# Optimization experiments

Hardware: AMD Instinct MI355X
Metric: run time of the kernel (lower is better)

The kernel has to match this reference:

```python
import jax, jax.numpy as jnp
import numpy as np

N = 100000      # nodes
E = 3200000     # edges
F_IN = 9        # atom features
H = 128         # hidden_dim
L = 4           # num_layers
G = 512         # graphs in batch
BN_EPS = 1e-5


def setup_inputs() -> dict:
    key = jax.random.key(0)
    ks = jax.random.split(key, 24)
    s = 0.05
    inp = {}
    inp["x"] = jax.random.normal(ks[0], (N, F_IN), jnp.float32)
    inp["edge_index"] = jax.random.randint(ks[1], (2, E), 0, N, dtype=jnp.int64)
    inp["batch"] = jnp.sort(jax.random.randint(ks[2], (N,), 0, G, dtype=jnp.int64))
    # atom embedding
    inp["Wemb"] = jax.random.normal(ks[3], (F_IN, H), jnp.float32) * s
    inp["bemb"] = jnp.zeros((H,), jnp.float32)
    # per-layer GINConv params (stacked over L layers)
    inp["eps"] = jnp.zeros((L,), jnp.float32)  # train_eps=True, init 0
    inp["W1"] = jax.random.normal(ks[4], (L, H, 2 * H), jnp.float32) * s
    inp["b1"] = jnp.zeros((L, 2 * H), jnp.float32)
    inp["g1"] = jax.random.uniform(ks[5], (L, 2 * H), jnp.float32, 0.9, 1.1)
    inp["be1"] = jax.random.normal(ks[6], (L, 2 * H), jnp.float32) * s
    inp["m1"] = jax.random.normal(ks[7], (L, 2 * H), jnp.float32) * s
    inp["v1"] = jax.random.uniform(ks[8], (L, 2 * H), jnp.float32, 0.5, 1.5)
    inp["W2"] = jax.random.normal(ks[9], (L, 2 * H, H), jnp.float32) * s
    inp["b2"] = jnp.zeros((L, H), jnp.float32)
    # outer BatchNorm per layer
    inp["g2"] = jax.random.uniform(ks[10], (L, H), jnp.float32, 0.9, 1.1)
    inp["be2"] = jax.random.normal(ks[11], (L, H), jnp.float32) * s
    inp["m2"] = jax.random.normal(ks[12], (L, H), jnp.float32) * s
    inp["v2"] = jax.random.uniform(ks[13], (L, H), jnp.float32, 0.5, 1.5)
    return inp


def _bn(x, g, b, m, v):
    # eval-mode BatchNorm1d with running stats
    return g * (x - m) * jax.lax.rsqrt(v + BN_EPS) + b


def reference(x, edge_index, batch, Wemb, bemb, eps, W1, b1, g1, be1, m1, v1,
              W2, b2, g2, be2, m2, v2):
    h = x @ Wemb + bemb                                   # [N, H]
    src, dst = edge_index[0], edge_index[1]
    for i in range(L):
        # GIN aggregation: sum of neighbor (source) features into target
        agg = jax.ops.segment_sum(h[src], dst, num_segments=N)   # [N, H]
        z = (1.0 + eps[i]) * h + agg
        # MLP: Linear -> BN -> ReLU -> Linear
        z = jax.nn.relu(_bn(z @ W1[i] + b1[i], g1[i], be1[i], m1[i], v1[i]))
        h = z @ W2[i] + b2[i]
        # outer BN + ReLU (dropout skipped: eval mode)
        h = jax.nn.relu(_bn(h, g2[i], be2[i], m2[i], v2[i]))
    # global_mean_pool
    sums = jax.ops.segment_sum(h, batch, num_segments=G)          # [G, H]
    counts = jax.ops.segment_sum(jnp.ones((N, 1), h.dtype), batch,
                                 num_segments=G)                  # [G, 1]
    return sums / jnp.maximum(counts, 1.0)
```

## Files before the change

### kernel.cpp

```cpp
#include <hip/hip_runtime.h>
#include <stdint.h>

#define H 128
#define H2 256
#define NLAYERS 4
#define BN_EPS 1e-5f

#define BSHIFT 10
#define NPB 1024
#define NBC 98
#define PART_BATCH 2048
#define EPT 8

typedef __attribute__((ext_vector_type(4))) float f32x4;
typedef __attribute__((ext_vector_type(8))) short bhalf8;

__device__ __forceinline__ float bf2f(unsigned short u) {
    union { unsigned int i; float f; } v;
    v.i = ((unsigned int)u) << 16;
    return v.f;
}
__device__ __forceinline__ unsigned short f2bf(float f) {
    union { float f; unsigned int i; } v;
    v.f = f;
    unsigned int b = v.i + 0x7FFFu + ((v.i >> 16) & 1u);
    return (unsigned short)(b >> 16);
}

__global__ __launch_bounds__(256) void embed_kernel(
    const float* __restrict__ x, const float* __restrict__ Wemb,
    const float* __restrict__ bemb, unsigned short* __restrict__ h, int N) {
    int n = blockIdx.x * 2 + (threadIdx.x >> 7);
    int f = threadIdx.x & 127;
    if (n >= N) return;
    const float* xr = x + (size_t)n * 9;
    float acc = bemb[f];
#pragma unroll
    for (int k = 0; k < 9; k++) acc += xr[k] * Wemb[k * H + f];
    h[(size_t)n * H + f] = f2bf(acc);
}

__global__ void prep_params(
    const float* __restrict__ b1, const float* __restrict__ g1, const float* __restrict__ be1,
    const float* __restrict__ m1, const float* __restrict__ v1,
    const float* __restrict__ b2, const float* __restrict__ g2, const float* __restrict__ be2,
    const float* __restrict__ m2, const float* __restrict__ v2,
    float* __restrict__ sc1, float* __restrict__ sh1,
    float* __restrict__ sc2, float* __restrict__ sh2) {
    int t = threadIdx.x;
    if (t < NLAYERS * H2) {
        float s = g1[t] * rsqrtf(v1[t] + BN_EPS);
        sc1[t] = s;
        sh1[t] = (b1[t] - m1[t]) * s + be1[t];
    }
    if (t < NLAYERS * H) {
        float s = g2[t] * rsqrtf(v2[t] + BN_EPS);
        sc2[t] = s;
        sh2[t] = (b2[t] - m2[t]) * s + be2[t];
    }
}

__global__ __launch_bounds__(256) void prep_weights(
    const float* __restrict__ W1, const float* __restrict__ W2,
    unsigned short* __restrict__ W1F, unsigned short* __restrict__ W2F) {
    int idx = blockIdx.x * 256 + threadIdx.x;
    if (idx >= NLAYERS * H * H2) return;
    {
        int e = idx & 7;
        int lane = (idx >> 3) & 63;
        int ks = (idx >> 9) & 3;
        int c16 = (idx >> 11) & 15;
        int l = idx >> 15;
        int c = c16 * 16 + (lane & 15);
        int k = ks * 32 + (lane >> 4) * 8 + e;
        W1F[idx] = f2bf(W1[((size_t)l * H + k) * H2 + c]);
    }
    {
        int e = idx & 7;
        int lane = (idx >> 3) & 63;
        int ks = (idx >> 9) & 7;
        int c16 = (idx >> 12) & 7;
        int l = idx >> 15;
        int c = c16 * 16 + (lane & 15);
        int k = ks * 32 + (lane >> 4) * 8 + e;
        W2F[idx] = f2bf(W2[((size_t)l * H2 + k) * H + c]);
    }
}

__global__ __launch_bounds__(256) void hist_coarse(const int* __restrict__ ei,
                                                   unsigned* __restrict__ bc_cnt,
                                                   int E, int nbc) {
    __shared__ unsigned lh[NBC];
    for (int i = threadIdx.x; i < nbc; i += 256) lh[i] = 0;
    __syncthreads();
    for (int e = blockIdx.x * 256 + threadIdx.x; e < E; e += gridDim.x * 256)
        atomicAdd(&lh[(unsigned)ei[E + e] >> BSHIFT], 1u);
    __syncthreads();
    for (int i = threadIdx.x; i < nbc; i += 256)
        if (lh[i]) atomicAdd(&bc_cnt[i], lh[i]);
}

__global__ __launch_bounds__(128) void scan_coarse(const unsigned* __restrict__ bc_cnt,
                                                   unsigned* __restrict__ bc_base,
                                                   unsigned* __restrict__ bc_cursor,
                                                   int nbc, int E) {
    __shared__ unsigned sd[128];
    int t = threadIdx.x;
    unsigned v = (t < nbc) ? bc_cnt[t] : 0u;
    sd[t] = v;
    __syncthreads();
    for (int off = 1; off < 128; off <<= 1) {
        unsigned xv = (t >= off) ? sd[t - off] : 0u;
        __syncthreads();
        sd[t] += xv;
        __syncthreads();
    }
    unsigned excl = sd[t] - v;
    if (t < nbc) {
        bc_base[t] = excl;
        bc_cursor[t] = excl;
    }
    if (t == 0) bc_base[nbc] = (unsigned)E;
}

__global__ __launch_bounds__(256) void partition_kernel(const int* __restrict__ ei,
                                                        unsigned* __restrict__ bc_cursor,
                                                        uint2* __restrict__ part,
                                                        int E, int nbc) {
    __shared__ unsigned lh[NBC];
    __shared__ unsigned lb[NBC];
    for (int i = threadIdx.x; i < nbc; i += 256) lh[i] = 0;
    __syncthreads();
    int base = blockIdx.x * PART_BATCH;
    int s[EPT], d[EPT];
    unsigned rank[EPT];
    int bk[EPT];
#pragma unroll
    for (int k = 0; k < EPT; k++) {
        int e = base + k * 256 + threadIdx.x;
        if (e < E) {
            s[k] = ei[e];
            d[k] = ei[E + e];
            bk[k] = (unsigned)d[k] >> BSHIFT;
            rank[k] = atomicAdd(&lh[bk[k]], 1u);
        } else bk[k] = -1;
    }
    __syncthreads();
    for (int i = threadIdx.x; i < nbc; i += 256)
        lb[i] = lh[i] ? atomicAdd(&bc_cursor[i], lh[i]) : 0u;
    __syncthreads();
#pragma unroll
    for (int k = 0; k < EPT; k++) {
        if (bk[k] >= 0) {
            unsigned p = lb[bk[k]] + rank[k];
            part[p] = make_uint2((unsigned)s[k], (unsigned)d[k]);
        }
    }
}

__global__ __launch_bounds__(1024) void bucket_degrees(const uint2* __restrict__ part,
                                                       const unsigned* __restrict__ bc_base,
                                                       unsigned* __restrict__ gdeg, int N) {
    __shared__ unsigned deg[NPB];
    int b = blockIdx.x;
    deg[threadIdx.x] = 0;
    __syncthreads();
    unsigned r0 = bc_base[b], r1 = bc_base[b + 1];
    for (unsigned i = r0 + threadIdx.x; i < r1; i += 1024)
        atomicAdd(&deg[part[i].y & (NPB - 1)], 1u);
    __syncthreads();
    int node = (b << BSHIFT) + threadIdx.x;
    if (node < N) gdeg[node] = deg[threadIdx.x];
}

__global__ __launch_bounds__(256) void scanA_kernel(const unsigned* __restrict__ deg,
                                                    unsigned* __restrict__ rowptr,
                                                    unsigned* __restrict__ bsum, int N) {
    __shared__ unsigned sd[256];
    int tid = threadIdx.x;
    int base = blockIdx.x * 1024 + tid * 4;
    unsigned v[4];
    unsigned s = 0;
#pragma unroll
    for (int j = 0; j < 4; j++) {
        v[j] = (base + j < N) ? deg[base + j] : 0u;
        s += v[j];
    }
    sd[tid] = s;
    __syncthreads();
    for (int off = 1; off < 256; off <<= 1) {
        unsigned xv = (tid >= off) ? sd[tid - off] : 0u;
        __syncthreads();
        sd[tid] += xv;
        __syncthreads();
    }
    unsigned excl = sd[tid] - s;
#pragma unroll
    for (int j = 0; j < 4; j++) {
        if (base + j < N) rowptr[base + j] = excl;
        excl += v[j];
    }
    if (tid == 255) bsum[blockIdx.x] = sd[255];
}

__global__ __launch_bounds__(1024) void scanB_kernel(unsigned* __restrict__ bsum, int nb) {
    __shared__ unsigned sd[1024];
    int t = threadIdx.x;
    unsigned s = (t < nb) ? bsum[t] : 0u;
    sd[t] = s;
    __syncthreads();
    for (int off = 1; off < 1024; off <<= 1) {
        unsigned xv = (t >= off) ? sd[t - off] : 0u;
        __syncthreads();
        sd[t] += xv;
        __syncthreads();
    }
    if (t < nb) bsum[t] = sd[t] - s;
}

__global__ __launch_bounds__(256) void scanC_kernel(unsigned* __restrict__ rowptr,
                                                    const unsigned* __restrict__ bsum,
                                                    int N, int E) {
    int base = blockIdx.x * 1024 + threadIdx.x * 4;
    unsigned off = bsum[blockIdx.x];
#pragma unroll
    for (int j = 0; j < 4; j++) {
        int i = base + j;
        if (i < N) rowptr[i] += off;
    }
    if (blockIdx.x == 0 && threadIdx.x == 0) rowptr[N] = (unsigned)E;
}

__global__ __launch_bounds__(1024) void bucket_fill(const uint2* __restrict__ part,
                                                    const unsigned* __restrict__ bc_base,
                                                    const unsigned* __restrict__ rowptr,
                                                    unsigned* __restrict__ col, int N) {
    __shared__ unsigned cur[NPB];
    int b = blockIdx.x;
    int node = (b << BSHIFT) + threadIdx.x;
    cur[threadIdx.x] = (node < N) ? rowptr[node] : 0u;
    __syncthreads();
    unsigned r0 = bc_base[b], r1 = bc_base[b + 1];
    for (unsigned i = r0 + threadIdx.x; i < r1; i += 1024) {
        uint2 e = part[i];
        unsigned p = atomicAdd(&cur[e.y & (NPB - 1)], 1u);
        col[p] = e.x;
    }
}

__global__ __launch_bounds__(256) void agg_kernel(
    const unsigned short* __restrict__ h, const unsigned* __restrict__ rowptr,
    const unsigned* __restrict__ col, const float* __restrict__ eps, int layer,
    unsigned short* __restrict__ z, int N) {
    int n = blockIdx.x * 4 + (threadIdx.x >> 6);
    if (n >= N) return;
    int lane = threadIdx.x & 63;
    int chunk = lane & 15;
    int sub = lane >> 4;
    unsigned r0 = rowptr[n], r1 = rowptr[n + 1];
    float a0[8], a1[8], a2[8], a3[8];
#pragma unroll
    for (int k = 0; k < 8; k++) { a0[k] = 0.f; a1[k] = 0.f; a2[k] = 0.f; a3[k] = 0.f; }
    unsigned j = r0 + sub;
    for (; j + 12 < r1; j += 16) {
        unsigned c0 = col[j], c1 = col[j + 4], c2 = col[j + 8], c3 = col[j + 12];
        bhalf8 v0 = *(const bhalf8*)&h[(size_t)c0 * H + chunk * 8];
        bhalf8 v1 = *(const bhalf8*)&h[(size_t)c1 * H + chunk * 8];
        bhalf8 v2 = *(const bhalf8*)&h[(size_t)c2 * H + chunk * 8];
        bhalf8 v3 = *(const bhalf8*)&h[(size_t)c3 * H + chunk * 8];
#pragma unroll
        for (int k = 0; k < 8; k++) {
            a0[k] += bf2f((unsigned short)v0[k]);
            a1[k] += bf2f((unsigned short)v1[k]);
            a2[k] += bf2f((unsigned short)v2[k]);
            a3[k] += bf2f((unsigned short)v3[k]);
        }
    }
    for (; j < r1; j += 4) {
        unsigned c0 = col[j];
        bhalf8 v0 = *(const bhalf8*)&h[(size_t)c0 * H + chunk * 8];
#pragma unroll
        for (int k = 0; k < 8; k++) a0[k] += bf2f((unsigned short)v0[k]);
    }
#pragma unroll
    for (int k = 0; k < 8; k++) {
        a0[k] += a1[k] + (a2[k] + a3[k]);
        a0[k] += __shfl_xor(a0[k], 16, 64);
        a0[k] += __shfl_xor(a0[k], 32, 64);
    }
    if (sub == 0) {
        float e = 1.0f + eps[layer];
        bhalf8 hv = *(const bhalf8*)&h[(size_t)n * H + chunk * 8];
        bhalf8 o;
#pragma unroll
        for (int k = 0; k < 8; k++)
            o[k] = (short)f2bf(e * bf2f((unsigned short)hv[k]) + a0[k]);
        *(bhalf8*)&z[(size_t)n * H + chunk * 8] = o;
    }
}

#define LDP 264
__global__ __launch_bounds__(256) void mlp_fused_kernel(
    const unsigned short* __restrict__ z, const unsigned short* __restrict__ W1F,
    const unsigned short* __restrict__ W2F,
    const float* __restrict__ sc1, const float* __restrict__ sh1,
    const float* __restrict__ sc2, const float* __restrict__ sh2,
    unsigned short* __restrict__ h, int N) {
    __shared__ unsigned short tl[64 * LDP];
    int wave = threadIdx.x >> 6, lane = threadIdx.x & 63;
    int rtile = blockIdx.x * 64;
    int rlane = lane & 15;
    int kq = lane >> 4;
    int kg = kq * 8;
    int arow[4];
#pragma unroll
    for (int rb = 0; rb < 4; rb++) {
        int r = rtile + rb * 16 + rlane;
        arow[rb] = r < N ? r : N - 1;
    }
    f32x4 zero = {0.f, 0.f, 0.f, 0.f};
    {
        f32x4 acc[4][4];
#pragma unroll
        for (int rb = 0; rb < 4; rb++)
#pragma unroll
            for (int cb = 0; cb < 4; cb++) acc[rb][cb] = zero;
#pragma unroll
        for (int ks = 0; ks < 4; ks++) {
            bhalf8 a[4], b[4];
#pragma unroll
            for (int rb = 0; rb < 4; rb++)
                a[rb] = *(const bhalf8*)&z[(size_t)arow[rb] * H + ks * 32 + kg];
#pragma unroll
            for (int cb = 0; cb < 4; cb++)
                b[cb] = *(const bhalf8*)&W1F[((size_t)((wave * 4 + cb) * 4 + ks) * 64 + lane) * 8];
#pragma unroll
            for (int rb = 0; rb < 4; rb++)
#pragma unroll
                for (int cb = 0; cb < 4; cb++)
                    acc[rb][cb] = __builtin_amdgcn_mfma_f32_16x16x32_bf16(a[rb], b[cb], acc[rb][cb], 0, 0, 0);
        }
#pragma unroll
        for (int cb = 0; cb < 4; cb++) {
            int colc = wave * 64 + cb * 16 + rlane;
            float sc = sc1[colc], sh = sh1[colc];
#pragma unroll
            for (int rb = 0; rb < 4; rb++) {
#pragma unroll
                for (int j = 0; j < 4; j++) {
                    int rl = rb * 16 + kq * 4 + j;
                    float vv = acc[rb][cb][j] * sc + sh;
                    vv = vv > 0.f ? vv : 0.f;
                    tl[rl * LDP + colc] = f2bf(vv);
                }
            }
        }
    }
    __syncthreads();
    {
        f32x4 acc[4][2];
#pragma unroll
        for (int rb = 0; rb < 4; rb++)
#pragma unroll
            for (int cb = 0; cb < 2; cb++) acc[rb][cb] = zero;
#pragma unroll
        for (int ks = 0; ks < 8; ks++) {
            bhalf8 a[4], b[2];
#pragma unroll
            for (int rb = 0; rb < 4; rb++)
                a[rb] = *(const bhalf8*)&tl[(rb * 16 + rlane) * LDP + ks * 32 + kg];
#pragma unroll
            for (int cb = 0; cb < 2; cb++)
                b[cb] = *(const bhalf8*)&W2F[((size_t)((wave * 2 + cb) * 8 + ks) * 64 + lane) * 8];
#pragma unroll
            for (int rb = 0; rb < 4; rb++)
#pragma unroll
                for (int cb = 0; cb < 2; cb++)
                    acc[rb][cb] = __builtin_amdgcn_mfma_f32_16x16x32_bf16(a[rb], b[cb], acc[rb][cb], 0, 0, 0);
        }
        int rr = rtile + kq * 4;
#pragma unroll
        for (int cb = 0; cb < 2; cb++) {
            int colc = wave * 32 + cb * 16 + rlane;
            float sc = sc2[colc], sh = sh2[colc];
#pragma unroll
            for (int rb = 0; rb < 4; rb++) {
#pragma unroll
                for (int j = 0; j < 4; j++) {
                    int row = rr + rb * 16 + j;
                    if (row < N) {
                        float vv = acc[rb][cb][j] * sc + sh;
                        vv = vv > 0.f ? vv : 0.f;
                        h[(size_t)row * H + colc] = f2bf(vv);
                    }
                }
            }
        }
    }
}

__global__ __launch_bounds__(128) void pool_kernel(
    const unsigned short* __restrict__ h, const int* __restrict__ batch,
    float* __restrict__ out, int N, int G) {
    __shared__ int se[2];
    int g = blockIdx.x;
    if (threadIdx.x == 0) {
        int lo = 0, hi = N;
        while (lo < hi) {
            int mid = (lo + hi) >> 1;
            if (batch[mid] < g) lo = mid + 1; else hi = mid;
        }
        se[0] = lo;
        hi = N;
        while (lo < hi) {
            int mid = (lo + hi) >> 1;
            if (batch[mid] < g + 1) lo = mid + 1; else hi = mid;
        }
        se[1] = lo;
    }
    __syncthreads();
    int s = se[0], e = se[1];
    int f = threadIdx.x;
    float acc = 0.f;
    for (int r = s; r < e; ++r) acc += bf2f(h[(size_t)r * H + f]);
    int cnt = e - s;
    out[(size_t)g * H + f] = cnt > 0 ? acc / (float)cnt : 0.f;
}

extern "C" void kernel_launch(void* const* d_in, const int* in_sizes, int n_in,
                              void* d_out, int out_size, void* d_ws, size_t ws_size,
                              hipStream_t stream) {
    const float* x     = (const float*)d_in[0];
    const int*   ei    = (const int*)d_in[1];
    const int*   batch = (const int*)d_in[2];
    const float* Wemb  = (const float*)d_in[3];
    const float* bemb  = (const float*)d_in[4];
    const float* eps   = (const float*)d_in[5];
    const float* W1    = (const float*)d_in[6];
    const float* b1    = (const float*)d_in[7];
    const float* g1    = (const float*)d_in[8];
    const float* be1   = (const float*)d_in[9];
    const float* m1    = (const float*)d_in[10];
    const float* v1    = (const float*)d_in[11];
    const float* W2    = (const float*)d_in[12];
    const float* b2    = (const float*)d_in[13];
    const float* g2    = (const float*)d_in[14];
    const float* be2   = (const float*)d_in[15];
    const float* m2    = (const float*)d_in[16];
    const float* v2    = (const float*)d_in[17];

    int N = in_sizes[0] / 9;
    int E = in_sizes[1] / 2;
    int G = out_size / H;
    int nbc = (N + NPB - 1) >> BSHIFT;

    char* p = (char*)d_ws;
    auto alloc = [&](size_t bytes) -> char* {
        char* r = p;
        p += (bytes + 255) & ~(size_t)255;
        return r;
    };
    unsigned short* h   = (unsigned short*)alloc((size_t)N * H * 2);
    unsigned short* z   = (unsigned short*)alloc((size_t)N * H * 2);
    uint2*          part = (uint2*)alloc((size_t)E * 8);
    unsigned*       rowptr = (unsigned*)alloc((size_t)(N + 1) * 4);
    unsigned*       gdeg   = (unsigned*)alloc((size_t)N * 4);
    unsigned*       bsum   = (unsigned*)alloc(1024 * 4);
    unsigned*       col    = (unsigned*)alloc((size_t)E * 4);
    unsigned short* W1F = (unsigned short*)alloc((size_t)NLAYERS * H * H2 * 2);
    unsigned short* W2F = (unsigned short*)alloc((size_t)NLAYERS * H * H2 * 2);
    float* sc1 = (float*)alloc(NLAYERS * H2 * 4);
    float* sh1 = (float*)alloc(NLAYERS * H2 * 4);
    float* sc2 = (float*)alloc(NLAYERS * H * 4);
    float* sh2 = (float*)alloc(NLAYERS * H * 4);
    unsigned* bc_cnt    = (unsigned*)alloc((NBC + 2) * 4);
    unsigned* bc_base   = (unsigned*)alloc((NBC + 2) * 4);
    unsigned* bc_cursor = (unsigned*)alloc((NBC + 2) * 4);

    hipMemsetAsync(bc_cnt, 0, (NBC + 2) * 4, stream);
    prep_params<<<1, 1024, 0, stream>>>(b1, g1, be1, m1, v1, b2, g2, be2, m2, v2,
                                        sc1, sh1, sc2, sh2);
    prep_weights<<<(NLAYERS * H * H2 + 255) / 256, 256, 0, stream>>>(W1, W2, W1F, W2F);
    embed_kernel<<<(N + 1) / 2, 256, 0, stream>>>(x, Wemb, bemb, h, N);

    hist_coarse<<<512, 256, 0, stream>>>(ei, bc_cnt, E, nbc);
    scan_coarse<<<1, 128, 0, stream>>>(bc_cnt, bc_base, bc_cursor, nbc, E);
    partition_kernel<<<(E + PART_BATCH - 1) / PART_BATCH, 256, 0, stream>>>(
        ei, bc_cursor, part, E, nbc);
    bucket_degrees<<<nbc, 1024, 0, stream>>>(part, bc_base, gdeg, N);
    int nb = (N + 1023) / 1024;
    scanA_kernel<<<nb, 256, 0, stream>>>(gdeg, rowptr, bsum, N);
    scanB_kernel<<<1, 1024, 0, stream>>>(bsum, nb);
    scanC_kernel<<<nb, 256, 0, stream>>>(rowptr, bsum, N, E);
    bucket_fill<<<nbc, 1024, 0, stream>>>(part, bc_base, rowptr, col, N);

    for (int l = 0; l < NLAYERS; l++) {
        agg_kernel<<<(N + 3) / 4, 256, 0, stream>>>(h, rowptr, col, eps, l, z, N);
        mlp_fused_kernel<<<(N + 63) / 64, 256, 0, stream>>>(
            z, W1F + (size_t)l * H * H2, W2F + (size_t)l * H * H2,
            sc1 + l * H2, sh1 + l * H2, sc2 + l * H, sh2 + l * H, h, N);
    }
    pool_kernel<<<G, 128, 0, stream>>>(h, batch, (float*)d_out, N, G);
}
```

Measured before the change: 929.2 us.

## Pack partition entries into one word, reshape aggregation and pool kernels

Partition entries now store the source index shifted together with the local destination offset in one 32-bit word, which halves the bytes written and read while building the CSR. The aggregation kernel moves to 128-thread blocks with two accumulators and a single tail step, trading memory-level parallelism for lower register pressure and higher occupancy. The pooling kernel splits each graph's rows across two thread halves with unrolled accumulation and combines them in shared memory.

```diff
diff --git a/kernel.cpp b/kernel.cpp
--- a/kernel.cpp
+++ b/kernel.cpp
@@ -125,7 +125,7 @@
 
 __global__ __launch_bounds__(256) void partition_kernel(const int* __restrict__ ei,
                                                         unsigned* __restrict__ bc_cursor,
-                                                        uint2* __restrict__ part,
+                                                        unsigned* __restrict__ part,
                                                         int E, int nbc) {
     __shared__ unsigned lh[NBC];
     __shared__ unsigned lb[NBC];
@@ -153,12 +153,12 @@
     for (int k = 0; k < EPT; k++) {
         if (bk[k] >= 0) {
             unsigned p = lb[bk[k]] + rank[k];
-            part[p] = make_uint2((unsigned)s[k], (unsigned)d[k]);
-        }
-    }
-}
-
-__global__ __launch_bounds__(1024) void bucket_degrees(const uint2* __restrict__ part,
+            part[p] = ((unsigned)s[k] << BSHIFT) | ((unsigned)d[k] & (NPB - 1));
+        }
+    }
+}
+
+__global__ __launch_bounds__(1024) void bucket_degrees(const unsigned* __restrict__ part,
                                                        const unsigned* __restrict__ bc_base,
                                                        unsigned* __restrict__ gdeg, int N) {
     __shared__ unsigned deg[NPB];
@@ -167,7 +167,7 @@
     __syncthreads();
     unsigned r0 = bc_base[b], r1 = bc_base[b + 1];
     for (unsigned i = r0 + threadIdx.x; i < r1; i += 1024)
-        atomicAdd(&deg[part[i].y & (NPB - 1)], 1u);
+        atomicAdd(&deg[part[i] & (NPB - 1)], 1u);
     __syncthreads();
     int node = (b << BSHIFT) + threadIdx.x;
     if (node < N) gdeg[node] = deg[threadIdx.x];
@@ -231,7 +231,7 @@
     if (blockIdx.x == 0 && threadIdx.x == 0) rowptr[N] = (unsigned)E;
 }
 
-__global__ __launch_bounds__(1024) void bucket_fill(const uint2* __restrict__ part,
+__global__ __launch_bounds__(1024) void bucket_fill(const unsigned* __restrict__ part,
                                                     const unsigned* __restrict__ bc_base,
                                                     const unsigned* __restrict__ rowptr,
                                                     unsigned* __restrict__ col, int N) {
@@ -242,51 +242,47 @@
     __syncthreads();
     unsigned r0 = bc_base[b], r1 = bc_base[b + 1];
     for (unsigned i = r0 + threadIdx.x; i < r1; i += 1024) {
-        uint2 e = part[i];
-        unsigned p = atomicAdd(&cur[e.y & (NPB - 1)], 1u);
-        col[p] = e.x;
-    }
-}
-
-__global__ __launch_bounds__(256) void agg_kernel(
+        unsigned e = part[i];
+        unsigned p = atomicAdd(&cur[e & (NPB - 1)], 1u);
+        col[p] = e >> BSHIFT;
+    }
+}
+
+__global__ __launch_bounds__(128) void agg_kernel(
     const unsigned short* __restrict__ h, const unsigned* __restrict__ rowptr,
     const unsigned* __restrict__ col, const float* __restrict__ eps, int layer,
     unsigned short* __restrict__ z, int N) {
-    int n = blockIdx.x * 4 + (threadIdx.x >> 6);
+    int n = blockIdx.x * 2 + (threadIdx.x >> 6);
     if (n >= N) return;
     int lane = threadIdx.x & 63;
     int chunk = lane & 15;
     int sub = lane >> 4;
     unsigned r0 = rowptr[n], r1 = rowptr[n + 1];
-    float a0[8], a1[8], a2[8], a3[8];
-#pragma unroll
-    for (int k = 0; k < 8; k++) { a0[k] = 0.f; a1[k] = 0.f; a2[k] = 0.f; a3[k] = 0.f; }
+    float acc0[8], acc1[8];
+#pragma unroll
+    for (int k = 0; k < 8; k++) { acc0[k] = 0.f; acc1[k] = 0.f; }
     unsigned j = r0 + sub;
-    for (; j + 12 < r1; j += 16) {
-        unsigned c0 = col[j], c1 = col[j + 4], c2 = col[j + 8], c3 = col[j + 12];
+    for (; j + 4 < r1; j += 8) {
+        unsigned c0 = col[j], c1 = col[j + 4];
         bhalf8 v0 = *(const bhalf8*)&h[(size_t)c0 * H + chunk * 8];
         bhalf8 v1 = *(const bhalf8*)&h[(size_t)c1 * H + chunk * 8];
-        bhalf8 v2 = *(const bhalf8*)&h[(size_t)c2 * H + chunk * 8];
-        bhalf8 v3 = *(const bhalf8*)&h[(size_t)c3 * H + chunk * 8];
 #pragma unroll
         for (int k = 0; k < 8; k++) {
-            a0[k] += bf2f((unsigned short)v0[k]);
-            a1[k] += bf2f((unsigned short)v1[k]);
-            a2[k] += bf2f((unsigned short)v2[k]);
-            a3[k] += bf2f((unsigned short)v3[k]);
-        }
-    }
-    for (; j < r1; j += 4) {
+            acc0[k] += bf2f((unsigned short)v0[k]);
+            acc1[k] += bf2f((unsigned short)v1[k]);
+        }
+    }
+    if (j < r1) {
         unsigned c0 = col[j];
         bhalf8 v0 = *(const bhalf8*)&h[(size_t)c0 * H + chunk * 8];
 #pragma unroll
-        for (int k = 0; k < 8; k++) a0[k] += bf2f((unsigned short)v0[k]);
+        for (int k = 0; k < 8; k++) acc0[k] += bf2f((unsigned short)v0[k]);
     }
 #pragma unroll
     for (int k = 0; k < 8; k++) {
-        a0[k] += a1[k] + (a2[k] + a3[k]);
-        a0[k] += __shfl_xor(a0[k], 16, 64);
-        a0[k] += __shfl_xor(a0[k], 32, 64);
+        acc0[k] += acc1[k];
+        acc0[k] += __shfl_xor(acc0[k], 16, 64);
+        acc0[k] += __shfl_xor(acc0[k], 32, 64);
     }
     if (sub == 0) {
         float e = 1.0f + eps[layer];
@@ -294,7 +290,7 @@
         bhalf8 o;
 #pragma unroll
         for (int k = 0; k < 8; k++)
-            o[k] = (short)f2bf(e * bf2f((unsigned short)hv[k]) + a0[k]);
+            o[k] = (short)f2bf(e * bf2f((unsigned short)hv[k]) + acc0[k]);
         *(bhalf8*)&z[(size_t)n * H + chunk * 8] = o;
     }
 }
@@ -399,9 +395,10 @@
     }
 }
 
-__global__ __launch_bounds__(128) void pool_kernel(
+__global__ __launch_bounds__(256) void pool_kernel(
     const unsigned short* __restrict__ h, const int* __restrict__ batch,
     float* __restrict__ out, int N, int G) {
+    __shared__ float sacc[2][128];
     __shared__ int se[2];
     int g = blockIdx.x;
     if (threadIdx.x == 0) {
@@ -420,11 +417,24 @@
     }
     __syncthreads();
     int s = se[0], e = se[1];
-    int f = threadIdx.x;
-    float acc = 0.f;
-    for (int r = s; r < e; ++r) acc += bf2f(h[(size_t)r * H + f]);
-    int cnt = e - s;
-    out[(size_t)g * H + f] = cnt > 0 ? acc / (float)cnt : 0.f;
+    int f = threadIdx.x & 127;
+    int half = threadIdx.x >> 7;
+    float a0 = 0.f, a1 = 0.f, a2 = 0.f, a3 = 0.f;
+    int r = s + half;
+    for (; r + 6 < e; r += 8) {
+        a0 += bf2f(h[(size_t)r * H + f]);
+        a1 += bf2f(h[(size_t)(r + 2) * H + f]);
+        a2 += bf2f(h[(size_t)(r + 4) * H + f]);
+        a3 += bf2f(h[(size_t)(r + 6) * H + f]);
+    }
+    for (; r < e; r += 2) a0 += bf2f(h[(size_t)r * H + f]);
+    sacc[half][f] = (a0 + a1) + (a2 + a3);
+    __syncthreads();
+    if (half == 0) {
+        int cnt = e - s;
+        float v = sacc[0][f] + sacc[1][f];
+        out[(size_t)g * H + f] = cnt > 0 ? v / (float)cnt : 0.f;
+    }
 }
 
 extern "C" void kernel_launch(void* const* d_in, const int* in_sizes, int n_in,
@@ -462,7 +472,7 @@
     };
     unsigned short* h   = (unsigned short*)alloc((size_t)N * H * 2);
     unsigned short* z   = (unsigned short*)alloc((size_t)N * H * 2);
-    uint2*          part = (uint2*)alloc((size_t)E * 8);
+    unsigned*       part = (unsigned*)alloc((size_t)E * 4);
     unsigned*       rowptr = (unsigned*)alloc((size_t)(N + 1) * 4);
     unsigned*       gdeg   = (unsigned*)alloc((size_t)N * 4);
     unsigned*       bsum   = (unsigned*)alloc(1024 * 4);
@@ -495,10 +505,10 @@
     bucket_fill<<<nbc, 1024, 0, stream>>>(part, bc_base, rowptr, col, N);
 
     for (int l = 0; l < NLAYERS; l++) {
-        agg_kernel<<<(N + 3) / 4, 256, 0, stream>>>(h, rowptr, col, eps, l, z, N);
+        agg_kernel<<<(N + 1) / 2, 128, 0, stream>>>(h, rowptr, col, eps, l, z, N);
         mlp_fused_kernel<<<(N + 63) / 64, 256, 0, stream>>>(
             z, W1F + (size_t)l * H * H2, W2F + (size_t)l * H * H2,
             sc1 + l * H2, sh1 + l * H2, sc2 + l * H, sh2 + l * H, h, N);
     }
-    pool_kernel<<<G, 128, 0, stream>>>(h, batch, (float*)d_out, N, G);
-}
+    pool_kernel<<<G, 256, 0, stream>>>(h, batch, (float*)d_out, N, G);
+}
```

After: 853.1 us. -8.2%, faster.
